# Kernel tuning notes

Hardware: AMD Instinct MI355X
Metric: run time of the kernel (lower is better)

## Reference

```python
import jax, jax.numpy as jnp
import numpy as np

B, S, HID = 2, 2048, 2048
H, KV, D = 16, 8, 128
EPS = 1e-6


def _rope_embeds(B, S, D):
    # standard RoPE cos/sin table, concatenated along last dim: [B, S, D]
    pos = jnp.arange(S, dtype=jnp.float32)  # same positions per batch row
    inv_freq = 1.0 / (10000.0 ** (jnp.arange(0, D // 2, dtype=jnp.float32) * (2.0 / D)))
    ang = pos[:, None] * inv_freq[None, :]  # [S, D/2]
    pe = jnp.concatenate([jnp.cos(ang), jnp.sin(ang)], axis=-1)  # [S, D]
    return jnp.broadcast_to(pe[None], (B, S, D))


def setup_inputs() -> dict:
    key = jax.random.key(0)
    ks = jax.random.split(key, 5)
    scale = 0.02
    return {
        "x": jax.random.normal(ks[0], (B, S, HID), jnp.float32),
        "pos_embeds": _rope_embeds(B, S, D),
        "q_w": jax.random.normal(ks[1], (H * D, HID), jnp.float32) * scale,
        "k_w": jax.random.normal(ks[2], (KV * D, HID), jnp.float32) * scale,
        "v_w": jax.random.normal(ks[3], (KV * D, HID), jnp.float32) * scale,
        "o_w": jax.random.normal(ks[4], (HID, H * D), jnp.float32) * scale,
        "q_norm_w": jnp.ones((D,), jnp.float32),
        "k_norm_w": jnp.ones((D,), jnp.float32),
    }


def _rmsnorm(x, w):
    var = jnp.mean(jnp.square(x), axis=-1, keepdims=True)
    return x * jax.lax.rsqrt(var + EPS) * w


def _apply_rope(x, pos_embeds):
    # x: [B, S, h, D]; pos_embeds: [B, S, D] = cat(cos, sin)
    x1, x2 = jnp.split(x, 2, axis=-1)
    cos, sin = jnp.split(pos_embeds[:, :, None, :], 2, axis=-1)
    return jnp.concatenate([x1 * cos - x2 * sin, x1 * sin + x2 * cos], axis=-1)


def reference(x, pos_embeds, q_w, k_w, v_w, o_w, q_norm_w, k_norm_w):
    b, s, _ = x.shape
    q = _apply_rope(_rmsnorm((x @ q_w.T).reshape(b, s, H, D), q_norm_w), pos_embeds)
    k = _apply_rope(_rmsnorm((x @ k_w.T).reshape(b, s, KV, D), k_norm_w), pos_embeds)
    v = (x @ v_w.T).reshape(b, s, KV, D)
    # GQA: repeat kv heads to match query heads
    rep = H // KV
    k = jnp.repeat(k, rep, axis=2)
    v = jnp.repeat(v, rep, axis=2)
    scores = jnp.einsum("bqhd,bkhd->bhqk", q, k) * (1.0 / np.sqrt(D))
    causal = jnp.tril(jnp.ones((s, s), dtype=bool))
    scores = jnp.where(causal[None, None], scores, jnp.finfo(scores.dtype).min)
    attn = jax.nn.softmax(scores, axis=-1)
    out = jnp.einsum("bhqk,bkhd->bqhd", attn, v).reshape(b, s, H * D)
    return out @ o_w.T
```

## Files before the change

kernel.cpp:

```cpp
#include <hip/hip_runtime.h>
#include <hip/hip_bf16.h>

#define BATCH 2
#define SEQ   2048
#define HID   2048
#define NH    16
#define NKV   8
#define HD    128

typedef __bf16 bf16;
typedef bf16  bf16x8  __attribute__((ext_vector_type(8)));
typedef bf16  bf16x4  __attribute__((ext_vector_type(4)));
typedef float floatx4 __attribute__((ext_vector_type(4)));

typedef __attribute__((address_space(3))) void lds_void;
typedef const __attribute__((address_space(1))) void gmem_void;

__device__ inline void async16(const void* g, void* l) {
    __builtin_amdgcn_global_load_lds((gmem_void*)g, (lds_void*)l, 16, 0, 0);
}

#define XN  8388608u
#define QWN 4194304u
#define KWN 2097152u
#define VWN 2097152u
#define OWN 4194304u

__global__ __launch_bounds__(256) void cvt_all(bf16* __restrict__ dst,
                                               const float* __restrict__ x,
                                               const float* __restrict__ qw,
                                               const float* __restrict__ kw,
                                               const float* __restrict__ vw,
                                               const float* __restrict__ ow)
{
    const int blk = blockIdx.x;
    const float* src;
    size_t off;
    if (blk < 4096)      { src = x;  off = (size_t)blk * 2048; }
    else if (blk < 6144) { src = qw; off = (size_t)(blk - 4096) * 2048; }
    else if (blk < 7168) { src = kw; off = (size_t)(blk - 6144) * 2048; }
    else if (blk < 8192) { src = vw; off = (size_t)(blk - 7168) * 2048; }
    else                 { src = ow; off = (size_t)(blk - 8192) * 2048; }

    const int t = threadIdx.x * 8;
    const float4* p = (const float4*)(src + off + t);
    float4 u0 = p[0], u1 = p[1];
    bf16x8 v;
    v[0] = (bf16)u0.x; v[1] = (bf16)u0.y; v[2] = (bf16)u0.z; v[3] = (bf16)u0.w;
    v[4] = (bf16)u1.x; v[5] = (bf16)u1.y; v[6] = (bf16)u1.z; v[7] = (bf16)u1.w;
    *(bf16x8*)(dst + (size_t)blk * 2048 + t) = v;
}

__global__ __launch_bounds__(512) void gemm256_qkv(bf16* __restrict__ Cq,
                                                   const bf16* __restrict__ A,
                                                   const bf16* __restrict__ W)
{
    __shared__ bf16 As[2 * 256 * 64];
    __shared__ bf16 Ws[2 * 256 * 64];

    const int tid  = threadIdx.x;
    const int wv   = tid >> 6;
    const int lane = tid & 63;
    const int quad = lane >> 4;
    const int c    = lane & 15;

    int lin = blockIdx.y * gridDim.x + blockIdx.x;
    lin = (lin & 7) * 32 + (lin >> 3);
    const int m0 = (lin & 15) * 256;
    const int n0 = (lin >> 4) * 256;

    const int wm = (wv >> 2) * 128;
    const int wn = (wv & 3) * 64;

    const int srow = tid >> 3;
    const int scol = (((tid & 7) ^ ((tid >> 3) & 7))) * 8;
    const int rsw  = (c & 7) * 8;

    constexpr int K  = 2048;
    constexpr int NT = K / 64;

    floatx4 acc[8][4] = {};

    auto stage = [&](int kt, int sel) {
        const size_t ko = (size_t)kt * 64;
        bf16* Ab = &As[sel * 16384];
        bf16* Wb = &Ws[sel * 16384];
        #pragma unroll
        for (int l = 0; l < 4; ++l)
            async16(A + (size_t)(m0 + l * 64 + srow) * K + ko + scol,
                    Ab + l * 4096 + wv * 512);
        #pragma unroll
        for (int l = 0; l < 4; ++l)
            async16(W + (size_t)(n0 + l * 64 + srow) * K + ko + scol,
                    Wb + l * 4096 + wv * 512);
    };

    stage(0, 0);

    int sel = 0;
    for (int t = 0; t < NT; ++t) {
        __syncthreads();
        if (t + 1 < NT) stage(t + 1, sel ^ 1);

        const bf16* Ab = &As[sel * 16384];
        const bf16* Wb = &Ws[sel * 16384];
        #pragma unroll
        for (int ks = 0; ks < 2; ++ks) {
            const int ro = (ks * 32 + quad * 8) ^ rsw;
            bf16x8 af[8], bw[4];
            #pragma unroll
            for (int i = 0; i < 8; i++)
                af[i] = *(const bf16x8*)(Ab + (wm + i * 16 + c) * 64 + ro);
            #pragma unroll
            for (int j = 0; j < 4; j++)
                bw[j] = *(const bf16x8*)(Wb + (wn + j * 16 + c) * 64 + ro);
            __builtin_amdgcn_s_setprio(1);
            #pragma unroll
            for (int i = 0; i < 8; i++)
                #pragma unroll
                for (int j = 0; j < 4; j++)
                    acc[i][j] = __builtin_amdgcn_mfma_f32_16x16x32_bf16(af[i], bw[j], acc[i][j], 0, 0, 0);
            __builtin_amdgcn_s_setprio(0);
        }
        sel ^= 1;
    }

    const int b = m0 >> 11;
    if (n0 < 2048) {
        #pragma unroll
        for (int i = 0; i < 8; i++)
            #pragma unroll
            for (int j = 0; j < 4; j++)
                #pragma unroll
                for (int r = 0; r < 4; r++) {
                    int m = m0 + wm + i * 16 + quad * 4 + r;
                    int n = n0 + wn + j * 16 + c;
                    Cq[(size_t)m * 2048 + n] = (bf16)acc[i][j][r];
                }
    } else if (n0 < 3072) {
        bf16* Ck = Cq + XN;
        #pragma unroll
        for (int i = 0; i < 8; i++)
            #pragma unroll
            for (int j = 0; j < 4; j++)
                #pragma unroll
                for (int r = 0; r < 4; r++) {
                    int m = m0 + wm + i * 16 + quad * 4 + r;
                    int n = n0 - 2048 + wn + j * 16 + c;
                    Ck[(size_t)m * 1024 + n] = (bf16)acc[i][j][r];
                }
    } else {
        bf16* Cv = Cq + XN + QWN;
        #pragma unroll
        for (int j = 0; j < 4; j++) {
            int n = n0 - 3072 + wn + j * 16 + c;
            size_t base = ((size_t)b * 1024 + n) * 2048;
            #pragma unroll
            for (int i = 0; i < 8; i++) {
                int s0 = (m0 & 2047) + wm + i * 16 + quad * 4;
                bf16x4 v;
                #pragma unroll
                for (int r = 0; r < 4; r++) v[r] = (bf16)acc[i][j][r];
                *(bf16x4*)(&Cv[base + s0]) = v;
            }
        }
    }
}

template <int AMODE, int WMODE, int CMODE>
__global__ __launch_bounds__(256) void gemm128(void* __restrict__ Cp,
                                               const void* __restrict__ Ap,
                                               const void* __restrict__ Wp,
                                               int M, int N, int K)
{
    __shared__ bf16 As[128 * 64];
    __shared__ bf16 Ws[128 * 64];

    const int tid  = threadIdx.x;
    const int wv   = tid >> 6;
    const int lane = tid & 63;
    const int quad = lane >> 4;
    const int c    = lane & 15;

    const int nwg = gridDim.x * gridDim.y;
    int bx = blockIdx.x, by = blockIdx.y;
    if ((nwg & 7) == 0) {
        int lin = by * gridDim.x + bx;
        lin = (lin & 7) * (nwg >> 3) + (lin >> 3);
        bx = lin % gridDim.x;
        by = lin / gridDim.x;
    }
    const int m0 = bx * 128;
    const int n0 = by * 128;
    const int wm = (wv >> 1) * 64;
    const int wn = (wv & 1) * 64;

    const int arow   = lane >> 3;
    const int acolsw = (((lane & 7) ^ (lane >> 3))) * 8;
    const int wsw    = ((tid >> 3) & 7) * 8;
    const int rsw    = (c & 7) * 8;

    floatx4 acc[4][4] = {};

    for (int k0 = 0; k0 < K; k0 += 64) {
        if constexpr (AMODE == 0) {
            const float* A = (const float*)Ap;
            #pragma unroll
            for (int it = 0; it < 4; it++) {
                int row = it * 32 + (tid >> 3);
                int col = (tid & 7) * 8;
                const float4* p = (const float4*)(A + (size_t)(m0 + row) * K + k0 + col);
                float4 u0 = p[0], u1 = p[1];
                bf16x8 v;
                v[0] = (bf16)u0.x; v[1] = (bf16)u0.y; v[2] = (bf16)u0.z; v[3] = (bf16)u0.w;
                v[4] = (bf16)u1.x; v[5] = (bf16)u1.y; v[6] = (bf16)u1.z; v[7] = (bf16)u1.w;
                *(bf16x8*)(&As[row * 64 + (col ^ wsw)]) = v;
            }
        } else {
            const bf16* A = (const bf16*)Ap;
            #pragma unroll
            for (int ch = 0; ch < 4; ch++) {
                int row = wv * 32 + ch * 8 + arow;
                async16(A + (size_t)(m0 + row) * K + k0 + acolsw,
                        &As[(wv * 32 + ch * 8) * 64]);
            }
        }
        if constexpr (WMODE == 0) {
            const float* W = (const float*)Wp;
            #pragma unroll
            for (int it = 0; it < 4; it++) {
                int row = it * 32 + (tid >> 3);
                int col = (tid & 7) * 8;
                const float4* p = (const float4*)(W + (size_t)(n0 + row) * K + k0 + col);
                float4 u0 = p[0], u1 = p[1];
                bf16x8 v;
                v[0] = (bf16)u0.x; v[1] = (bf16)u0.y; v[2] = (bf16)u0.z; v[3] = (bf16)u0.w;
                v[4] = (bf16)u1.x; v[5] = (bf16)u1.y; v[6] = (bf16)u1.z; v[7] = (bf16)u1.w;
                *(bf16x8*)(&Ws[row * 64 + (col ^ wsw)]) = v;
            }
        } else {
            const bf16* W = (const bf16*)Wp;
            #pragma unroll
            for (int ch = 0; ch < 4; ch++) {
                int row = wv * 32 + ch * 8 + arow;
                async16(W + (size_t)(n0 + row) * K + k0 + acolsw,
                        &Ws[(wv * 32 + ch * 8) * 64]);
            }
        }
        __syncthreads();

        #pragma unroll
        for (int t = 0; t < 2; t++) {
            const int ro = (t * 32 + quad * 8) ^ rsw;
            bf16x8 af[4], bw[4];
            #pragma unroll
            for (int i = 0; i < 4; i++)
                af[i] = *(const bf16x8*)(&As[(wm + i * 16 + c) * 64 + ro]);
            #pragma unroll
            for (int j = 0; j < 4; j++)
                bw[j] = *(const bf16x8*)(&Ws[(wn + j * 16 + c) * 64 + ro]);
            #pragma unroll
            for (int i = 0; i < 4; i++)
                #pragma unroll
                for (int j = 0; j < 4; j++)
                    acc[i][j] = __builtin_amdgcn_mfma_f32_16x16x32_bf16(af[i], bw[j], acc[i][j], 0, 0, 0);
        }
        __syncthreads();
    }

    if constexpr (CMODE == 0) {
        float* C = (float*)Cp;
        #pragma unroll
        for (int i = 0; i < 4; i++)
            #pragma unroll
            for (int j = 0; j < 4; j++)
                #pragma unroll
                for (int r = 0; r < 4; r++) {
                    int m = m0 + wm + i * 16 + quad * 4 + r;
                    int n = n0 + wn + j * 16 + c;
                    C[(size_t)m * N + n] = acc[i][j][r];
                }
    } else if constexpr (CMODE == 1) {
        bf16* C = (bf16*)Cp;
        #pragma unroll
        for (int i = 0; i < 4; i++)
            #pragma unroll
            for (int j = 0; j < 4; j++)
                #pragma unroll
                for (int r = 0; r < 4; r++) {
                    int m = m0 + wm + i * 16 + quad * 4 + r;
                    int n = n0 + wn + j * 16 + c;
                    C[(size_t)m * N + n] = (bf16)acc[i][j][r];
                }
    } else if constexpr (CMODE == 2) {
        bf16* C = (bf16*)Cp;
        const int b = m0 >> 11;
        #pragma unroll
        for (int j = 0; j < 4; j++) {
            int n = n0 + wn + j * 16 + c;
            size_t base = ((size_t)b * N + n) * 2048;
            #pragma unroll
            for (int i = 0; i < 4; i++) {
                int s0 = (m0 & 2047) + wm + i * 16 + quad * 4;
                bf16x4 v;
                #pragma unroll
                for (int r = 0; r < 4; r++) v[r] = (bf16)acc[i][j][r];
                *(bf16x4*)(&C[base + s0]) = v;
            }
        }
    } else {
        bf16* Cq = (bf16*)Cp;
        if (n0 < 2048) {
            #pragma unroll
            for (int i = 0; i < 4; i++)
                #pragma unroll
                for (int j = 0; j < 4; j++)
                    #pragma unroll
                    for (int r = 0; r < 4; r++) {
                        int m = m0 + wm + i * 16 + quad * 4 + r;
                        int n = n0 + wn + j * 16 + c;
                        Cq[(size_t)m * 2048 + n] = (bf16)acc[i][j][r];
                    }
        } else if (n0 < 3072) {
            bf16* Ck = Cq + XN;
            #pragma unroll
            for (int i = 0; i < 4; i++)
                #pragma unroll
                for (int j = 0; j < 4; j++)
                    #pragma unroll
                    for (int r = 0; r < 4; r++) {
                        int m = m0 + wm + i * 16 + quad * 4 + r;
                        int n = n0 - 2048 + wn + j * 16 + c;
                        Ck[(size_t)m * 1024 + n] = (bf16)acc[i][j][r];
                    }
        } else {
            bf16* Cv = Cq + XN + QWN;
            const int b = m0 >> 11;
            #pragma unroll
            for (int j = 0; j < 4; j++) {
                int n = n0 - 3072 + wn + j * 16 + c;
                size_t base = ((size_t)b * 1024 + n) * 2048;
                #pragma unroll
                for (int i = 0; i < 4; i++) {
                    int s0 = (m0 & 2047) + wm + i * 16 + quad * 4;
                    bf16x4 v;
                    #pragma unroll
                    for (int r = 0; r < 4; r++) v[r] = (bf16)acc[i][j][r];
                    *(bf16x4*)(&Cv[base + s0]) = v;
                }
            }
        }
    }
}

__global__ __launch_bounds__(128) void norm_rope_k(bf16* __restrict__ k,
                                                   const float* __restrict__ pe,
                                                   const float* __restrict__ knw)
{
    const int s  = blockIdx.x;
    const int hh = blockIdx.y;
    const int b  = blockIdx.z;
    const int d  = threadIdx.x;

    bf16* buf = k + (size_t)(b * SEQ + s) * 1024 + hh * HD;

    float x = (float)buf[d];
    float ss = x * x;
    #pragma unroll
    for (int m = 32; m; m >>= 1) ss += __shfl_xor(ss, m);

    __shared__ float red[2];
    __shared__ float nv[128];
    if ((d & 63) == 0) red[d >> 6] = ss;
    __syncthreads();
    float var = (red[0] + red[1]) * (1.0f / 128.0f);
    float nx = x * rsqrtf(var + 1e-6f) * knw[d];
    nv[d] = nx;
    __syncthreads();

    const float* pev = pe + ((size_t)b * SEQ + s) * HD;
    float o;
    if (d < 64) {
        o = nx * pev[d] - nv[d + 64] * pev[64 + d];
    } else {
        o = nv[d - 64] * pev[d] + nx * pev[d - 64];
    }
    buf[d] = (bf16)o;
}

__global__ __launch_bounds__(512) void fattn(bf16* __restrict__ O,
                                             const bf16* __restrict__ Q,
                                             const bf16* __restrict__ Kh,
                                             const bf16* __restrict__ Vtg,
                                             const float* __restrict__ pe,
                                             const float* __restrict__ qnw)
{
    const int h    = blockIdx.z;
    const int b    = blockIdx.y;
    const int qblk = (h & 8) ? (int)blockIdx.x
                             : ((int)gridDim.x - 1 - (int)blockIdx.x);
    const int kv   = h >> 1;

    const int tid  = threadIdx.x;
    const int wv   = tid >> 6;
    const int lane = tid & 63;
    const int quad = lane >> 4;
    const int c    = lane & 15;

    __shared__ bf16 Ks[64 * 136];
    __shared__ bf16 Vs[128 * 72];
    __shared__ bf16 Ps[8 * 16 * 72];

    const int qw = qblk * 128 + wv * 16;

    bf16x8 qf[4];
    {
        const bf16* qp = Q + (size_t)(b * SEQ + qw + c) * 2048 + h * HD + quad * 8;
        float qv[4][8];
        float ss = 0.0f;
        #pragma unroll
        for (int t = 0; t < 4; t++) {
            bf16x8 raw = *(const bf16x8*)(qp + t * 32);
            #pragma unroll
            for (int j = 0; j < 8; j++) { qv[t][j] = (float)raw[j]; ss += qv[t][j] * qv[t][j]; }
        }
        ss += __shfl_xor(ss, 16);
        ss += __shfl_xor(ss, 32);
        const float inv = rsqrtf(ss * (1.0f / 128.0f) + 1e-6f);
        const float* pev = pe + (size_t)(b * SEQ + qw + c) * HD + quad * 8;
        float nx[4][8], pv[4][8];
        #pragma unroll
        for (int t = 0; t < 4; t++)
            #pragma unroll
            for (int j = 0; j < 8; j++) {
                pv[t][j] = pev[t * 32 + j];
                nx[t][j] = qv[t][j] * inv * qnw[t * 32 + quad * 8 + j];
            }
        #pragma unroll
        for (int t = 0; t < 2; t++)
            #pragma unroll
            for (int j = 0; j < 8; j++) {
                qf[t][j]     = (bf16)(nx[t][j] * pv[t][j]     - nx[t + 2][j] * pv[t + 2][j]);
                qf[t + 2][j] = (bf16)(nx[t][j] * pv[t + 2][j] + nx[t + 2][j] * pv[t][j]);
            }
    }

    floatx4 o_acc[8] = {};
    float l_part[4] = {};

    const bf16* kbase = Kh  + (size_t)b * SEQ * 1024 + kv * HD;
    const bf16* vbase = Vtg + ((size_t)b * 1024 + kv * HD) * 2048;

    const int kr  = tid >> 3, ksc = (tid & 7) * 16;
    const int vd  = tid >> 2, vkc = (tid & 3) * 16;
    bf16* psw = &Ps[wv * 16 * 72];
    const int nkt = 2 * qblk + 2;
    const float kS = 0.08838834764831845f * 1.4426950408889634f;
    const float kB = 11.5f * 1.4426950408889634f;

    bf16x8 kreg[2], vreg[2];
    {
        const bf16* kp = kbase + (size_t)kr * 1024 + ksc;
        const bf16* vp = vbase + (size_t)vd * 2048 + vkc;
        kreg[0] = *(const bf16x8*)(kp);
        kreg[1] = *(const bf16x8*)(kp + 8);
        vreg[0] = *(const bf16x8*)(vp);
        vreg[1] = *(const bf16x8*)(vp + 8);
    }

    for (int kt = 0; kt < nkt; kt++) {
        const int k0 = kt * 64;
        *(bf16x8*)(&Ks[kr * 136 + ksc])     = kreg[0];
        *(bf16x8*)(&Ks[kr * 136 + ksc + 8]) = kreg[1];
        *(bf16x8*)(&Vs[vd * 72 + vkc])      = vreg[0];
        *(bf16x8*)(&Vs[vd * 72 + vkc + 8])  = vreg[1];
        __syncthreads();

        if (kt + 1 < nkt) {
            const bf16* kp = kbase + (size_t)(k0 + 64 + kr) * 1024 + ksc;
            const bf16* vp = vbase + (size_t)vd * 2048 + (k0 + 64) + vkc;
            kreg[0] = *(const bf16x8*)(kp);
            kreg[1] = *(const bf16x8*)(kp + 8);
            vreg[0] = *(const bf16x8*)(vp);
            vreg[1] = *(const bf16x8*)(vp + 8);
        }

        if (k0 <= qw + 15) {
            floatx4 sc[4] = {};
            #pragma unroll
            for (int t = 0; t < 4; t++) {
                #pragma unroll
                for (int g = 0; g < 4; g++) {
                    bf16x8 kf = *(const bf16x8*)(&Ks[(g * 16 + c) * 136 + t * 32 + quad * 8]);
                    sc[g] = __builtin_amdgcn_mfma_f32_16x16x32_bf16(qf[t], kf, sc[g], 0, 0, 0);
                }
            }

            const bool tail = (kt >= nkt - 2);
            #pragma unroll
            for (int r = 0; r < 4; r++) {
                const int qrow = qw + quad * 4 + r;
                #pragma unroll
                for (int g = 0; g < 4; g++) {
                    float p = exp2f(sc[g][r] * kS - kB);
                    if (tail && (k0 + g * 16 + c > qrow)) p = 0.0f;
                    l_part[r] += p;
                    psw[(quad * 4 + r) * 72 + g * 16 + c] = (bf16)p;
                }
            }
            asm volatile("s_waitcnt lgkmcnt(0)" ::: "memory");
            bf16x8 pf0 = *(const bf16x8*)(&psw[c * 72 + quad * 8]);
            bf16x8 pf1 = *(const bf16x8*)(&psw[c * 72 + 32 + quad * 8]);

            #pragma unroll
            for (int f = 0; f < 8; f++) {
                bf16x8 vf0 = *(const bf16x8*)(&Vs[(f * 16 + c) * 72 + quad * 8]);
                bf16x8 vf1 = *(const bf16x8*)(&Vs[(f * 16 + c) * 72 + 32 + quad * 8]);
                o_acc[f] = __builtin_amdgcn_mfma_f32_16x16x32_bf16(pf0, vf0, o_acc[f], 0, 0, 0);
                o_acc[f] = __builtin_amdgcn_mfma_f32_16x16x32_bf16(pf1, vf1, o_acc[f], 0, 0, 0);
            }
        }
        __syncthreads();
    }

    #pragma unroll
    for (int r = 0; r < 4; r++) {
        float l = l_part[r];
        #pragma unroll
        for (int msk = 8; msk; msk >>= 1) l += __shfl_xor(l, msk);
        const float inv = 1.0f / l;
        bf16* op = O + (size_t)(b * SEQ + qw + quad * 4 + r) * 2048 + h * HD;
        #pragma unroll
        for (int f = 0; f < 8; f++) op[f * 16 + c] = (bf16)(o_acc[f][r] * inv);
    }
}

extern "C" void kernel_launch(void* const* d_in, const int* in_sizes, int n_in,
                              void* d_out, int out_size, void* d_ws, size_t ws_size,
                              hipStream_t stream)
{
    const float* x   = (const float*)d_in[0];
    const float* pe  = (const float*)d_in[1];
    const float* qw  = (const float*)d_in[2];
    const float* kw  = (const float*)d_in[3];
    const float* vw  = (const float*)d_in[4];
    const float* ow  = (const float*)d_in[5];
    const float* qnw = (const float*)d_in[6];
    const float* knw = (const float*)d_in[7];
    float* out = (float*)d_out;

    bf16* qb = (bf16*)d_ws;
    bf16* kb = qb + XN;
    bf16* vt = kb + KWN * 2;
    bf16* ab = vt + VWN * 2;
    bf16* cvt_base = ab + XN;

    const bool fit = ws_size >= (size_t)92274688;
    const int M = BATCH * SEQ;

    if (fit) {
        bf16* xb  = cvt_base;
        bf16* qwb = xb  + XN;
        bf16* owb = qwb + QWN + KWN + VWN;

        cvt_all<<<10240, 256, 0, stream>>>(xb, x, qw, kw, vw, ow);

        gemm256_qkv<<<dim3(16, 16), 512, 0, stream>>>(qb, xb, qwb);

        norm_rope_k<<<dim3(SEQ, NKV, BATCH), 128, 0, stream>>>(kb, pe, knw);
        fattn<<<dim3(SEQ / 128, BATCH, NH), 512, 0, stream>>>(ab, qb, kb, vt, pe, qnw);

        gemm128<1, 1, 0><<<dim3(32, 16), 256, 0, stream>>>(out, ab, owb, M, 2048, 2048);
    } else {
        gemm128<0, 0, 1><<<dim3(32, 16), 256, 0, stream>>>(qb, x, qw, M, 2048, 2048);
        gemm128<0, 0, 1><<<dim3(32,  8), 256, 0, stream>>>(kb, x, kw, M, 1024, 2048);
        gemm128<0, 0, 2><<<dim3(32,  8), 256, 0, stream>>>(vt, x, vw, M, 1024, 2048);

        norm_rope_k<<<dim3(SEQ, NKV, BATCH), 128, 0, stream>>>(kb, pe, knw);
        fattn<<<dim3(SEQ / 128, BATCH, NH), 512, 0, stream>>>(ab, qb, kb, vt, pe, qnw);

        gemm128<0, 0, 0><<<dim3(32, 16), 256, 0, stream>>>(out, ab, ow, M, 2048, 2048);
    }
}
```

Before: 335.3 us.

## Double-buffer K/V LDS tiles with XOR swizzle to drop one barrier per iteration

Replaces the padded K/V/P shared-memory layouts with unpadded XOR-swizzled layouts and double-buffers the K and V tiles. The next tile is written into the alternate buffer after compute, so the trailing __syncthreads per iteration goes away. The intent is to cut barrier stalls and LDS bank conflicts in the attention inner loop. The cost is roughly double the LDS for K/V, which may lower occupancy, and the swizzle indexing has to be correct on both the write and read sides.

```diff
diff --git a/kernel.cpp b/kernel.cpp
--- a/kernel.cpp
+++ b/kernel.cpp
@@ -407,9 +407,9 @@
     const int quad = lane >> 4;
     const int c    = lane & 15;
 
-    __shared__ bf16 Ks[64 * 136];
-    __shared__ bf16 Vs[128 * 72];
-    __shared__ bf16 Ps[8 * 16 * 72];
+    __shared__ bf16 Ks[2 * 64 * 128];
+    __shared__ bf16 Vs[2 * 128 * 64];
+    __shared__ bf16 Ps[8 * 16 * 64];
 
     const int qw = qblk * 128 + wv * 16;
 
@@ -453,7 +453,11 @@
 
     const int kr  = tid >> 3, ksc = (tid & 7) * 16;
     const int vd  = tid >> 2, vkc = (tid & 3) * 16;
-    bf16* psw = &Ps[wv * 16 * 72];
+    const int kx  = (kr & 7) * 8;
+    const int vx  = (vd & 7) * 8;
+    const int rx  = (c & 7) * 8;
+    const int px  = ((quad & 1) * 4) * 8;
+    bf16* psw = &Ps[wv * 16 * 64];
     const int nkt = 2 * qblk + 2;
     const float kS = 0.08838834764831845f * 1.4426950408889634f;
     const float kB = 11.5f * 1.4426950408889634f;
@@ -467,13 +471,14 @@
         vreg[0] = *(const bf16x8*)(vp);
         vreg[1] = *(const bf16x8*)(vp + 8);
     }
-
+    *(bf16x8*)(&Ks[kr * 128 + (ksc ^ kx)])       = kreg[0];
+    *(bf16x8*)(&Ks[kr * 128 + ((ksc + 8) ^ kx)]) = kreg[1];
+    *(bf16x8*)(&Vs[vd * 64 + (vkc ^ vx)])        = vreg[0];
+    *(bf16x8*)(&Vs[vd * 64 + ((vkc + 8) ^ vx)])  = vreg[1];
+
+    int sel = 0;
     for (int kt = 0; kt < nkt; kt++) {
         const int k0 = kt * 64;
-        *(bf16x8*)(&Ks[kr * 136 + ksc])     = kreg[0];
-        *(bf16x8*)(&Ks[kr * 136 + ksc + 8]) = kreg[1];
-        *(bf16x8*)(&Vs[vd * 72 + vkc])      = vreg[0];
-        *(bf16x8*)(&Vs[vd * 72 + vkc + 8])  = vreg[1];
         __syncthreads();
 
         if (kt + 1 < nkt) {
@@ -485,13 +490,17 @@
             vreg[1] = *(const bf16x8*)(vp + 8);
         }
 
+        const bf16* Kb = &Ks[sel * 8192];
+        const bf16* Vb = &Vs[sel * 8192];
+
         if (k0 <= qw + 15) {
             floatx4 sc[4] = {};
             #pragma unroll
             for (int t = 0; t < 4; t++) {
+                const int ro = (t * 32 + quad * 8) ^ rx;
                 #pragma unroll
                 for (int g = 0; g < 4; g++) {
-                    bf16x8 kf = *(const bf16x8*)(&Ks[(g * 16 + c) * 136 + t * 32 + quad * 8]);
+                    bf16x8 kf = *(const bf16x8*)(&Kb[(g * 16 + c) * 128 + ro]);
                     sc[g] = __builtin_amdgcn_mfma_f32_16x16x32_bf16(qf[t], kf, sc[g], 0, 0, 0);
                 }
             }
@@ -500,27 +509,37 @@
             #pragma unroll
             for (int r = 0; r < 4; r++) {
                 const int qrow = qw + quad * 4 + r;
+                const int xw = px + r * 8;
                 #pragma unroll
                 for (int g = 0; g < 4; g++) {
                     float p = exp2f(sc[g][r] * kS - kB);
                     if (tail && (k0 + g * 16 + c > qrow)) p = 0.0f;
                     l_part[r] += p;
-                    psw[(quad * 4 + r) * 72 + g * 16 + c] = (bf16)p;
+                    psw[(quad * 4 + r) * 64 + ((g * 16 + c) ^ xw)] = (bf16)p;
                 }
             }
             asm volatile("s_waitcnt lgkmcnt(0)" ::: "memory");
-            bf16x8 pf0 = *(const bf16x8*)(&psw[c * 72 + quad * 8]);
-            bf16x8 pf1 = *(const bf16x8*)(&psw[c * 72 + 32 + quad * 8]);
+            bf16x8 pf0 = *(const bf16x8*)(&psw[c * 64 + ((quad * 8) ^ rx)]);
+            bf16x8 pf1 = *(const bf16x8*)(&psw[c * 64 + ((32 + quad * 8) ^ rx)]);
 
             #pragma unroll
             for (int f = 0; f < 8; f++) {
-                bf16x8 vf0 = *(const bf16x8*)(&Vs[(f * 16 + c) * 72 + quad * 8]);
-                bf16x8 vf1 = *(const bf16x8*)(&Vs[(f * 16 + c) * 72 + 32 + quad * 8]);
+                bf16x8 vf0 = *(const bf16x8*)(&Vb[(f * 16 + c) * 64 + ((quad * 8) ^ rx)]);
+                bf16x8 vf1 = *(const bf16x8*)(&Vb[(f * 16 + c) * 64 + ((32 + quad * 8) ^ rx)]);
                 o_acc[f] = __builtin_amdgcn_mfma_f32_16x16x32_bf16(pf0, vf0, o_acc[f], 0, 0, 0);
                 o_acc[f] = __builtin_amdgcn_mfma_f32_16x16x32_bf16(pf1, vf1, o_acc[f], 0, 0, 0);
             }
         }
-        __syncthreads();
+
+        if (kt + 1 < nkt) {
+            bf16* Kc = &Ks[(sel ^ 1) * 8192];
+            bf16* Vc = &Vs[(sel ^ 1) * 8192];
+            *(bf16x8*)(&Kc[kr * 128 + (ksc ^ kx)])       = kreg[0];
+            *(bf16x8*)(&Kc[kr * 128 + ((ksc + 8) ^ kx)]) = kreg[1];
+            *(bf16x8*)(&Vc[vd * 64 + (vkc ^ vx)])        = vreg[0];
+            *(bf16x8*)(&Vc[vd * 64 + ((vkc + 8) ^ vx)])  = vreg[1];
+        }
+        sel ^= 1;
     }
 
     #pragma unroll
```

Measured after the change: 359.1 us. 7.1% more time.
